# Optimization experiments

Measured on AMD Instinct MI355X. Metric: run time of the kernel, lower is better.

Reference implementation:

```python
import jax, jax.numpy as jnp
import numpy as np

L, H, DH, C, NRBF = 2, 4, 16, 64, 16   # depth, heads, dim_head, hidden dim, radial basis size
R = 10.0                                # valid_radius
EPS = 1e-8


def _layernorm(x, g, b):
    m = x.mean(-1, keepdims=True)
    v = ((x - m) ** 2).mean(-1, keepdims=True)
    return (x - m) / jnp.sqrt(v + 1e-5) * g + b


def setup_inputs() -> dict:
    key = jax.random.key(0)
    ks = iter(jax.random.split(key, 48))
    B, N, IN, OUT = 16, 128, 11, 19
    def rn(shape, fan_in):
        return jax.random.normal(next(ks), shape, jnp.float32) * (fan_in ** -0.5)
    inp = {
        "feats": jax.random.normal(next(ks), (B, N, IN), jnp.float32),
        "coords": jax.random.normal(next(ks), (B, N, 3), jnp.float32) * 3.0,
        "W_emb": rn((IN, C), IN), "b_emb": jnp.zeros((C,), jnp.float32),
        "Wq0": rn((L, C, H * DH), C), "Wk0": rn((L, C, H * DH), C), "Wv0": rn((L, C, H * DH), C),
        "Wq1": rn((L, C, H * DH), C), "Wk1": rn((L, C, H * DH), C), "Wv1": rn((L, C, H * DH), C),
        "rW1": rn((L, NRBF, 32), NRBF), "rb1": jnp.zeros((L, 32), jnp.float32),
        "rW2": rn((L, 32, 4 * H), 32), "rb2": jnp.zeros((L, 4 * H), jnp.float32),
        "Wo0": rn((L, H * DH, C), H * DH), "bo0": jnp.zeros((L, C), jnp.float32),
        "Wo1": rn((L, H * DH, C), H * DH),
        "g0": jnp.ones((L, C), jnp.float32), "b0": jnp.zeros((L, C), jnp.float32),
        "gn": jnp.ones((L, C), jnp.float32), "bn": jnp.zeros((L, C), jnp.float32),
        "g2": jnp.ones((L, C), jnp.float32), "b2": jnp.zeros((L, C), jnp.float32),
        "F1": rn((L, C, 4 * C), C), "fb1": jnp.zeros((L, 4 * C), jnp.float32),
        "F2": rn((L, 4 * C, C), 4 * C), "fb2": jnp.zeros((L, C), jnp.float32),
        "Wf1": rn((L, C, C), C),
        "Wout": rn((C, OUT), C), "bout": jnp.zeros((OUT,), jnp.float32),
        "mask": jnp.ones((B, N), bool),
        "adj": jnp.zeros((B, N, N), bool),
    }
    return inp


def reference(feats, coords, W_emb, b_emb, Wq0, Wk0, Wv0, Wq1, Wk1, Wv1,
              rW1, rb1, rW2, rb2, Wo0, bo0, Wo1, g0, b0, gn, bn, g2, b2,
              F1, fb1, F2, fb2, Wf1, Wout, bout, mask, adj):
    B, N = mask.shape
    f0 = feats @ W_emb + b_emb                                   # [B,N,C] degree-0 feats
    f1 = jnp.zeros((B, N, C, 3), f0.dtype)                       # degree-1 feats
    rel = coords[:, None, :, :] - coords[:, :, None, :]          # [B,N,N,3] r_j - r_i
    dist = jnp.sqrt((rel ** 2).sum(-1) + EPS)                    # [B,N,N]
    Y1 = rel / dist[..., None]                                   # degree-1 spherical harmonic
    pairm = mask[:, None, :] & mask[:, :, None]
    nmask = ((dist <= R) | adj) & pairm & (~jnp.eye(N, dtype=bool))
    centers = jnp.linspace(0.0, R, NRBF).astype(f0.dtype)
    rbf = jnp.exp(-((dist[..., None] - centers) ** 2) / (2.0 * (R / NRBF) ** 2))  # [B,N,N,NRBF]
    nmf = nmask[:, None].astype(f0.dtype)                        # [B,1,N,N]
    scale = DH ** -0.5

    for l in range(L):
        # radial kernel weights for the four tensor-product paths (per head)
        rh = jax.nn.relu(rbf @ rW1[l] + rb1[l])
        w = (rh @ rW2[l] + rb2[l]).reshape(B, N, N, 4, H)
        w = jnp.moveaxis(w, -1, 1)                               # [B,H,N,N,4]
        w00, w01, w10, w11 = w[..., 0], w[..., 1], w[..., 2], w[..., 3]

        x0 = _layernorm(f0, g0[l], b0[l])
        def heads0(x, W):
            return (x @ W).reshape(B, N, H, DH).transpose(0, 2, 1, 3)          # [B,H,N,DH]
        def heads1(x, W):
            return jnp.einsum('bncv,cm->bnmv', x, W).reshape(B, N, H, DH, 3).transpose(0, 2, 1, 3, 4)
        q0, k0, v0 = heads0(x0, Wq0[l]), heads0(x0, Wk0[l]), heads0(x0, Wv0[l])
        q1, k1, v1 = heads1(f1, Wq1[l]), heads1(f1, Wk1[l]), heads1(f1, Wv1[l])

        # invariant attention logits from degree-0 and degree-1 channels
        sim = (jnp.einsum('bhid,bhjd->bhij', q0, k0) * w00
               + jnp.einsum('bhidv,bhjdv->bhij', q1, k1) * w11) * scale
        sim = jnp.where(nmask[:, None], sim, -1e9)
        a = jax.nn.softmax(sim, axis=-1) * nmf                   # zero rows w/o neighbors

        # equivariant messages: 0->0, 1->0 (dot with Y1), 0->1 (times Y1), 1->1
        out0 = (jnp.einsum('bhij,bhjd->bhid', a * w00, v0)
                + jnp.einsum('bhij,bhjdv,bijv->bhid', a * w10, v1, Y1))
        out1 = (jnp.einsum('bhij,bhjd,bijv->bhidv', a * w01, v0, Y1)
                + jnp.einsum('bhij,bhjdv->bhidv', a * w11, v1))

        f0 = f0 + out0.transpose(0, 2, 1, 3).reshape(B, N, H * DH) @ Wo0[l] + bo0[l]
        f1 = f1 + jnp.einsum('bnmv,mc->bncv',
                             out1.transpose(0, 2, 1, 3, 4).reshape(B, N, H * DH, 3), Wo1[l])

        # equivariant norm on degree-1 (phase * learned gate of the norm)
        n1 = jnp.sqrt((f1 ** 2).sum(-1) + EPS)                   # [B,N,C]
        f1 = f1 / n1[..., None] * jax.nn.relu(n1 * gn[l] + bn[l])[..., None]

        # feedforward: MLP on degree-0, channel-mixing linear on degree-1
        f0 = f0 + jax.nn.relu(_layernorm(f0, g2[l], b2[l]) @ F1[l] + fb1[l]) @ F2[l] + fb2[l]
        f1 = f1 + jnp.einsum('bncv,cd->bndv', f1, Wf1[l])

    mf = mask.astype(f0.dtype)
    pooled = (f0 * mf[..., None]).sum(1) / jnp.clip(mf.sum(1, keepdims=True), 1.0, None)
    return pooled @ Wout + bout
```

## Files before the change

### kernel.cpp

```cpp
#include <hip/hip_runtime.h>
#include <hip/hip_bf16.h>


typedef __hip_bfloat16 bf16;
typedef __attribute__((ext_vector_type(8))) short short8;
typedef __attribute__((ext_vector_type(4))) float float4v;

__device__ __forceinline__ float waveSum64(float v) {
#pragma unroll
  for (int m = 1; m < 64; m <<= 1) v += __shfl_xor(v, m, 64);
  return v;
}

__device__ __forceinline__ float bits2f(unsigned short b) {
  return __uint_as_float(((unsigned int)b) << 16);
}
__device__ __forceinline__ unsigned short f2bu(float f) {
  unsigned int u = __float_as_uint(f);
  u = (u + 0x7fffu + ((u >> 16) & 1u)) >> 16;
  return (unsigned short)u;
}
__device__ __forceinline__ short8 pack8(float4 a, float4 b) {
  short8 r;
  r[0] = (short)f2bu(a.x); r[1] = (short)f2bu(a.y);
  r[2] = (short)f2bu(a.z); r[3] = (short)f2bu(a.w);
  r[4] = (short)f2bu(b.x); r[5] = (short)f2bu(b.y);
  r[6] = (short)f2bu(b.z); r[7] = (short)f2bu(b.w);
  return r;
}

__device__ __forceinline__ int voteSlice(const unsigned short* u, int start, int stride) {
  int insane = 0;
  for (int e = start; e < 1024; e += stride) {
    float f = bits2f(u[2 * e]);
    float af = fabsf(f);
    insane += (!(af < 1e4f) || (f != 0.f && af < 1e-20f)) ? 1 : 0;
  }
  return insane;
}

__device__ __forceinline__ float ldraw(const void* src, int idx, bool isbf) {
  if (isbf) return bits2f(((const unsigned short*)src)[idx]);
  return ((const float*)src)[idx];
}

struct ConvArgs {
  const void* src[30];
  int off[31];
};

__global__ void k_convtab(ConvArgs a, float* dst, int total, int nconv,
                          float2* __restrict__ tab) {
  __shared__ int cnt;
  int tid = threadIdx.x;
  if (tid == 0) cnt = 0;
  __syncthreads();
  atomicAdd(&cnt, voteSlice((const unsigned short*)a.src[0], tid, 256));
  __syncthreads();
  bool isbf = (cnt <= 100);

  if ((int)blockIdx.x < nconv) {
    int e = blockIdx.x * 256 + tid;
    if (e >= total) return;
    int k = 0;
    while (k < 29 && a.off[k + 1] <= e) k++;
    dst[e] = ldraw(a.src[k], e - a.off[k], isbf);
    return;
  }
  int g = (blockIdx.x - nconv) * 256 + tid;
  int l = g >> 10, bin = g & 1023;
  __shared__ float sW1[512], sb1[32], sW2[512], sb2[16];
  for (int k = tid; k < 512; k += 256) {
    sW1[k] = ldraw(a.src[10], l * 512 + k, isbf);
    sW2[k] = ldraw(a.src[12], l * 512 + k, isbf);
  }
  if (tid < 32) sb1[tid] = ldraw(a.src[11], l * 32 + tid, isbf);
  if (tid < 16) sb2[tid] = ldraw(a.src[13], l * 16 + tid, isbf);
  __syncthreads();
  float w[2][16];
#pragma unroll
  for (int t = 0; t < 2; ++t) {
    float d = (float)(bin + t) * 0.01f;
    float rbf[16];
#pragma unroll
    for (int r = 0; r < 16; ++r) {
      float x = d - (10.0f / 15.0f) * (float)r;
      rbf[r] = __expf(-x * x * 1.28f);
    }
#pragma unroll
    for (int o = 0; o < 16; ++o) w[t][o] = sb2[o];
    for (int k = 0; k < 32; ++k) {
      float acc = sb1[k];
#pragma unroll
      for (int r = 0; r < 16; ++r) acc += rbf[r] * sW1[r * 32 + k];
      acc = fmaxf(acc, 0.f);
#pragma unroll
      for (int o = 0; o < 16; ++o) w[t][o] += acc * sW2[k * 16 + o];
    }
  }
#pragma unroll
  for (int o = 0; o < 16; ++o)
    tab[l * 16384 + bin * 16 + o] = make_float2(w[0][o], w[1][o]);
}

__global__ void k_proj0(const float* __restrict__ feats, const float* __restrict__ W_emb,
                        const float* __restrict__ b_emb, const float* __restrict__ g0,
                        const float* __restrict__ b0, const float* __restrict__ Wq0,
                        const float* __restrict__ Wk0, const float* __restrict__ Wv0,
                        float* __restrict__ f0, float* __restrict__ q0,
                        float* __restrict__ k0, float* __restrict__ v0) {
  int row = blockIdx.x;
  int b = row >> 7, n = row & 127;
  int m = threadIdx.x;
  __shared__ float fs[11], x0s[64];
  if (m < 11) fs[m] = feats[row * 11 + m];
  __syncthreads();
  float val = b_emb[m];
#pragma unroll
  for (int k = 0; k < 11; k++) val += fs[k] * W_emb[k * 64 + m];
  f0[row * 64 + m] = val;
  float mu = waveSum64(val) * (1.f / 64.f);
  float dv = val - mu;
  float var = waveSum64(dv * dv) * (1.f / 64.f);
  x0s[m] = dv * rsqrtf(var + 1e-5f) * g0[m] + b0[m];
  __syncthreads();
  float aq = 0, ak = 0, av = 0;
  for (int c = 0; c < 64; c++) {
    float x = x0s[c];
    aq += x * Wq0[c * 64 + m];
    ak += x * Wk0[c * 64 + m];
    av += x * Wv0[c * 64 + m];
  }
  int h = m >> 4, d = m & 15;
  size_t o0 = ((size_t)((b * 4 + h) * 128 + n)) * 16 + d;
  q0[o0] = aq; k0[o0] = ak; v0[o0] = av;
}

__global__ void k_proj(const float* __restrict__ f0, const float* __restrict__ f1,
                       const float* __restrict__ g0, const float* __restrict__ b0,
                       const float* __restrict__ Wq0, const float* __restrict__ Wk0,
                       const float* __restrict__ Wv0, const float* __restrict__ Wq1,
                       const float* __restrict__ Wk1, const float* __restrict__ Wv1,
                       float* __restrict__ q0, float* __restrict__ k0, float* __restrict__ v0,
                       float* __restrict__ q1, float* __restrict__ k1, float* __restrict__ v1,
                       int l) {
  int row = blockIdx.x;
  int b = row >> 7, n = row & 127;
  int m = threadIdx.x;
  __shared__ float x0s[64], f1s[192];
  float val = f0[row * 64 + m];
  float mu = waveSum64(val) * (1.f / 64.f);
  float dv = val - mu;
  float var = waveSum64(dv * dv) * (1.f / 64.f);
  float xn = dv * rsqrtf(var + 1e-5f) * g0[l * 64 + m] + b0[l * 64 + m];
  x0s[m] = xn;
  f1s[m * 3 + 0] = f1[row * 192 + m * 3 + 0];
  f1s[m * 3 + 1] = f1[row * 192 + m * 3 + 1];
  f1s[m * 3 + 2] = f1[row * 192 + m * 3 + 2];
  __syncthreads();
  const float* wq0 = Wq0 + l * 4096;
  const float* wk0 = Wk0 + l * 4096;
  const float* wv0 = Wv0 + l * 4096;
  const float* wq1 = Wq1 + l * 4096;
  const float* wk1 = Wk1 + l * 4096;
  const float* wv1 = Wv1 + l * 4096;
  float aq = 0, ak = 0, av = 0;
  float aq1x = 0, aq1y = 0, aq1z = 0, ak1x = 0, ak1y = 0, ak1z = 0, av1x = 0, av1y = 0, av1z = 0;
  for (int c = 0; c < 64; c++) {
    float x = x0s[c];
    aq += x * wq0[c * 64 + m];
    ak += x * wk0[c * 64 + m];
    av += x * wv0[c * 64 + m];
    float fx = f1s[c * 3 + 0], fy = f1s[c * 3 + 1], fz = f1s[c * 3 + 2];
    float w;
    w = wq1[c * 64 + m]; aq1x += fx * w; aq1y += fy * w; aq1z += fz * w;
    w = wk1[c * 64 + m]; ak1x += fx * w; ak1y += fy * w; ak1z += fz * w;
    w = wv1[c * 64 + m]; av1x += fx * w; av1y += fy * w; av1z += fz * w;
  }
  int h = m >> 4, d = m & 15;
  size_t o0 = ((size_t)((b * 4 + h) * 128 + n)) * 16 + d;
  size_t o1 = ((size_t)((b * 4 + h) * 128 + n)) * 48 + d * 3;
  q0[o0] = aq; k0[o0] = ak; v0[o0] = av;
  q1[o1 + 0] = aq1x; q1[o1 + 1] = aq1y; q1[o1 + 2] = aq1z;
  k1[o1 + 0] = ak1x; k1[o1 + 1] = ak1y; k1[o1 + 2] = ak1z;
  v1[o1 + 0] = av1x; v1[o1 + 1] = av1y; v1[o1 + 2] = av1z;
}

template <int HASF1>
__global__ void __launch_bounds__(256, 4) k_attn(
    const float* __restrict__ coords, const float2* __restrict__ tab,
    const float* __restrict__ q0, const float* __restrict__ k0,
    const float* __restrict__ v0, const float* __restrict__ q1,
    const float* __restrict__ k1, const float* __restrict__ v1,
    float* __restrict__ out0, float* __restrict__ out1) {
  __shared__ union {
    unsigned short ks[128][64];
    unsigned short A16[64][128];
  } U;
  __shared__ unsigned int S01[8][128];
  __shared__ unsigned short Bt[64][128];
  __shared__ float cs[3][128];

  int tid = threadIdx.x;
  int bid = blockIdx.x;
  int bh = bid & 63, it = bid >> 6;
  int h = bh & 3, b = bh >> 2;
  int ibase = it * 8;
  size_t rowbase = (size_t)bh * 128;
  int lane = tid & 63, waveid = tid >> 6;
  int ln = lane & 15, lg = lane >> 4;

  short8 P0f = {0, 0, 0, 0, 0, 0, 0, 0};
  short8 P1f = {0, 0, 0, 0, 0, 0, 0, 0};
  short8 P2f = {0, 0, 0, 0, 0, 0, 0, 0};
  if (ln < 8) {
    int i = ibase + ln;
    if (HASF1) {
      const float* q1p = q1 + (rowbase + i) * 48;
      float4 fa = *(const float4*)&q1p[lg * 8];
      float4 fb = *(const float4*)&q1p[lg * 8 + 4];
      P0f = pack8(fa, fb);
      if (lg < 2) {
        fa = *(const float4*)&q1p[32 + lg * 8];
        fb = *(const float4*)&q1p[32 + lg * 8 + 4];
        P1f = pack8(fa, fb);
      }
    }
    if (lg >= 2) {
      const float* q0p = q0 + (rowbase + i) * 16;
      float4 fa = *(const float4*)&q0p[(lg - 2) * 8];
      float4 fb = *(const float4*)&q0p[(lg - 2) * 8 + 4];
      P2f = pack8(fa, fb);
    }
  }

  if (HASF1) {
    for (int e = tid; e < 2048; e += 256) {
      int j = e >> 4, t0 = (e & 15) * 4;
      float4 f;
      if (t0 < 48) f = *(const float4*)&k1[(rowbase + j) * 48 + t0];
      else f = *(const float4*)&k0[(rowbase + j) * 16 + (t0 - 48)];
      int g = t0 >> 3;
      ushort4 pk = {f2bu(f.x), f2bu(f.y), f2bu(f.z), f2bu(f.w)};
      *(ushort4*)&U.ks[j][((g ^ (j & 7)) << 3) | (t0 & 7)] = pk;
    }
  } else {
    for (int e = tid; e < 1024; e += 256) {
      int j = e >> 3, t0 = 32 + (e & 7) * 4;
      ushort4 pk = {0, 0, 0, 0};
      if (t0 >= 48) {
        float4 f = *(const float4*)&k0[(rowbase + j) * 16 + (t0 - 48)];
        pk.x = f2bu(f.x); pk.y = f2bu(f.y); pk.z = f2bu(f.z); pk.w = f2bu(f.w);
      }
      int g = t0 >> 3;
      *(ushort4*)&U.ks[j][((g ^ (j & 7)) << 3) | (t0 & 7)] = pk;
    }
  }
  for (int e = tid; e < 512; e += 256) {
    int j = e >> 2, q = e & 3;
    float4 f = *(const float4*)&v0[(rowbase + j) * 16 + q * 4];
    int jhi = j >> 3, jl = j & 7;
#pragma unroll
    for (int i2 = 0; i2 < 4; ++i2) {
      int d = q * 4 + i2;
      int sl = (jhi ^ d) << 3;
      float fv = (i2 == 0) ? f.x : (i2 == 1) ? f.y : (i2 == 2) ? f.z : f.w;
      Bt[d][sl | jl] = f2bu(fv);
      if (!HASF1) {
        Bt[16 + d][sl | jl] = 0;
        Bt[32 + d][sl | jl] = 0;
        Bt[48 + d][sl | jl] = 0;
      }
    }
  }
  if (HASF1) {
    for (int e = tid; e < 1536; e += 256) {
      int j = e / 12, q = e - j * 12;
      float4 f = *(const float4*)&v1[(rowbase + j) * 48 + q * 4];
      int jhi = j >> 3, jl = j & 7;
#pragma unroll
      for (int i2 = 0; i2 < 4; ++i2) {
        int flat = q * 4 + i2;
        int d = flat / 3, vv = flat - d * 3;
        int sl = (jhi ^ d) << 3;
        float fv = (i2 == 0) ? f.x : (i2 == 1) ? f.y : (i2 == 2) ? f.z : f.w;
        Bt[(vv + 1) * 16 + d][sl | jl] = f2bu(fv);
      }
    }
  }
  if (tid < 128) {
    cs[0][tid] = coords[((size_t)b * 128 + tid) * 3 + 0];
    cs[1][tid] = coords[((size_t)b * 128 + tid) * 3 + 1];
    cs[2][tid] = coords[((size_t)b * 128 + tid) * 3 + 2];
  }
  __syncthreads();

#pragma unroll
  for (int q = 0; q < 2; ++q) {
    int j = (waveid * 2 + q) * 16 + ln;
    int swz = j & 7;
    short8 bk1 = *(const short8*)&U.ks[j][(((4 + lg) ^ swz) << 3)];
    float4v a0 = {0.f, 0.f, 0.f, 0.f};
    a0 = __builtin_amdgcn_mfma_f32_16x16x32_bf16(P2f, bk1, a0, 0, 0, 0);
    float4v a1 = {0.f, 0.f, 0.f, 0.f};
    if (HASF1) {
      short8 bk0 = *(const short8*)&U.ks[j][((lg ^ swz) << 3)];
      a1 = __builtin_amdgcn_mfma_f32_16x16x32_bf16(P0f, bk0, a1, 0, 0, 0);
      a1 = __builtin_amdgcn_mfma_f32_16x16x32_bf16(P1f, bk1, a1, 0, 0, 0);
    }
    if (lg < 2) {
#pragma unroll
      for (int r = 0; r < 4; ++r) {
        unsigned int pk =
            (unsigned int)f2bu(a0[r]) | ((unsigned int)f2bu(a1[r]) << 16);
        S01[lg * 4 + r][j] = pk;
      }
    }
  }
  __syncthreads();

  {
    int row = tid >> 5, jg = tid & 31;
    int i = ibase + row;
    float cix = cs[0][i], ciy = cs[1][i], ciz = cs[2][i];
    uint4 sv = *(const uint4*)&S01[row][jg * 4];
    float e4[4], w4[4][4], yv[4][3];
    int nmmask = 0;
    float mx = -3e38f;
#pragma unroll
    for (int jj = 0; jj < 4; ++jj) {
      int j = jg * 4 + jj;
      float rx = cs[0][j] - cix;
      float ry = cs[1][j] - ciy;
      float rz = cs[2][j] - ciz;
      float dd = sqrtf(rx * rx + ry * ry + rz * rz + 1e-8f);
      float inv = 1.f / dd;
      yv[jj][0] = rx * inv; yv[jj][1] = ry * inv; yv[jj][2] = rz * inv;
      float tt = fminf(dd, 10.229f) * 100.f;
      int i0 = (int)tt;
      float fr = tt - (float)i0;
      const float2* Tp = tab + (i0 << 4) + h;
      float2 t0 = Tp[0], t1 = Tp[4], t2 = Tp[8], t3 = Tp[12];
      w4[jj][0] = t0.x + fr * (t0.y - t0.x);
      w4[jj][1] = t1.x + fr * (t1.y - t1.x);
      w4[jj][2] = t2.x + fr * (t2.y - t2.x);
      w4[jj][3] = t3.x + fr * (t3.y - t3.x);
      unsigned int sw = (jj == 0) ? sv.x : (jj == 1) ? sv.y : (jj == 2) ? sv.z : sv.w;
      float s0j = bits2f((unsigned short)(sw & 0xffffu));
      float s1j = bits2f((unsigned short)(sw >> 16));
      float sim = (s0j * w4[jj][0] + (HASF1 ? s1j * w4[jj][3] : 0.f)) * 0.25f;
      bool nm = (dd <= 10.0f) && (j != i);
      if (nm) nmmask |= (1 << jj);
      sim = nm ? sim : -1e9f;
      e4[jj] = sim;
      mx = fmaxf(mx, sim);
    }
#pragma unroll
    for (int m = 1; m < 32; m <<= 1) mx = fmaxf(mx, __shfl_xor(mx, m, 64));
    float ssum = 0.f;
#pragma unroll
    for (int jj = 0; jj < 4; ++jj) {
      e4[jj] = __expf(e4[jj] - mx);
      ssum += e4[jj];
    }
#pragma unroll
    for (int m = 1; m < 32; m <<= 1) ssum += __shfl_xor(ssum, m, 64);
    float rinv = 1.f / ssum;
    float aj[4];
#pragma unroll
    for (int jj = 0; jj < 4; ++jj)
      aj[jj] = ((nmmask >> jj) & 1) ? e4[jj] * rinv : 0.f;
#pragma unroll
    for (int s = 0; s < 8; ++s) {
      unsigned short t4[4];
#pragma unroll
      for (int jj = 0; jj < 4; ++jj) {
        float v;
        if (s == 0) v = aj[jj] * w4[jj][0];
        else if (s < 4) v = aj[jj] * w4[jj][2] * yv[jj][s - 1];
        else if (s < 7) v = aj[jj] * w4[jj][1] * yv[jj][s - 4];
        else v = aj[jj] * w4[jj][3];
        t4[jj] = f2bu(v);
      }
      ushort4 pk = {t4[0], t4[1], t4[2], t4[3]};
      int arow = row * 8 + s;
      int g = jg >> 1;
      *(ushort4*)&U.A16[arow][(((g ^ (arow & 15)) << 3) | ((jg & 1) * 4))] = pk;
    }
  }
  __syncthreads();

  float4v acc[4];
#pragma unroll
  for (int nt = 0; nt < 4; ++nt) acc[nt] = (float4v){0.f, 0.f, 0.f, 0.f};
  int m = waveid * 16 + ln;
#pragma unroll
  for (int kst = 0; kst < 4; ++kst) {
    int gk = kst * 4 + lg;
    short8 af = *(const short8*)&U.A16[m][((gk ^ ln) << 3)];
#pragma unroll
    for (int nt = 0; nt < 4; ++nt) {
      short8 bf = *(const short8*)&Bt[nt * 16 + ln][((gk ^ ln) << 3)];
      acc[nt] = __builtin_amdgcn_mfma_f32_16x16x32_bf16(af, bf, acc[nt], 0, 0, 0);
    }
  }
  {
    int qr = waveid * 2 + (lg >> 1);
    size_t orow = rowbase + ibase + qr;
    if ((lg & 1) == 0) {
      out0[orow * 16 + ln] = acc[0][0] + acc[1][1] + acc[2][2] + acc[3][3];
    } else {
#pragma unroll
      for (int vv = 0; vv < 3; ++vv)
        out1[orow * 48 + ln * 3 + vv] = acc[0][vv] + acc[1 + vv][3];
    }
  }
}

template <int LZ>
__global__ void __launch_bounds__(256) k_postff(
    const float* __restrict__ Wo0, const float* __restrict__ bo0,
    const float* __restrict__ Wo1, const float* __restrict__ gn,
    const float* __restrict__ bn, const float* __restrict__ g2,
    const float* __restrict__ b2w, const float* __restrict__ F1,
    const float* __restrict__ fb1, const float* __restrict__ F2,
    const float* __restrict__ fb2, const float* __restrict__ Wf1,
    const float* __restrict__ out0, const float* __restrict__ out1,
    float* __restrict__ f0, float* __restrict__ f1, int l) {
  int row = blockIdx.x;
  int b = row >> 7, n = row & 127;
  int tid = threadIdx.x;
  int g = tid >> 6, c = tid & 63;
  __shared__ float o0s[64], o1s[192], rs[64], xnl[64], hb[256], f1g[192];
  __shared__ float p0[4][64];
  __shared__ float p1[4][3][64];

  if (tid < 64) {
    int h = tid >> 4, d = tid & 15;
    o0s[tid] = out0[((size_t)((b * 4 + h) * 128 + n)) * 16 + d];
  } else {
    int t = tid - 64;
    int cc = t / 3, v = t - cc * 3;
    int h = cc >> 4, d = cc & 15;
    o1s[t] = out1[((size_t)((b * 4 + h) * 128 + n)) * 48 + d * 3 + v];
  }
  __syncthreads();
  {
    const float* wo0 = Wo0 + l * 4096;
    const float* wo1 = Wo1 + l * 4096;
    float a0 = 0, ax = 0, ay = 0, az = 0;
#pragma unroll
    for (int mi = 0; mi < 16; ++mi) {
      int m = g * 16 + mi;
      a0 += o0s[m] * wo0[m * 64 + c];
      float w = wo1[m * 64 + c];
      ax += o1s[m * 3 + 0] * w;
      ay += o1s[m * 3 + 1] * w;
      az += o1s[m * 3 + 2] * w;
    }
    p0[g][c] = a0;
    p1[g][0][c] = ax; p1[g][1][c] = ay; p1[g][2][c] = az;
  }
  __syncthreads();
  if (tid < 64) {
    float a0 = bo0[l * 64 + c] + p0[0][c] + p0[1][c] + p0[2][c] + p0[3][c];
    float f0p = f0[row * 64 + c] + a0;
    rs[c] = f0p;
    float fx = p1[0][0][c] + p1[1][0][c] + p1[2][0][c] + p1[3][0][c];
    float fy = p1[0][1][c] + p1[1][1][c] + p1[2][1][c] + p1[3][1][c];
    float fz = p1[0][2][c] + p1[1][2][c] + p1[2][2][c] + p1[3][2][c];
    if (!LZ) {
      fx += f1[row * 192 + c * 3 + 0];
      fy += f1[row * 192 + c * 3 + 1];
      fz += f1[row * 192 + c * 3 + 2];
    }
    float n1 = sqrtf(fx * fx + fy * fy + fz * fz + 1e-8f);
    float gate = fmaxf(n1 * gn[l * 64 + c] + bn[l * 64 + c], 0.f);
    float sc = gate / n1;
    f1g[c * 3 + 0] = fx * sc;
    f1g[c * 3 + 1] = fy * sc;
    f1g[c * 3 + 2] = fz * sc;
    float mu = waveSum64(f0p) * (1.f / 64.f);
    float dv = f0p - mu;
    float var = waveSum64(dv * dv) * (1.f / 64.f);
    xnl[c] = dv * rsqrtf(var + 1e-5f) * g2[l * 64 + c] + b2w[l * 64 + c];
  }
  __syncthreads();
  {
    float a = fb1[l * 256 + tid];
    const float* Fp = F1 + l * 16384;
    for (int cc = 0; cc < 64; ++cc) a += xnl[cc] * Fp[cc * 256 + tid];
    hb[tid] = fmaxf(a, 0.f);
  }
  __syncthreads();
  {
    const float* Fp = F2 + l * 16384;
    float s = 0;
#pragma unroll 8
    for (int kk = 0; kk < 64; ++kk) {
      int k = g * 64 + kk;
      s += hb[k] * Fp[k * 64 + c];
    }
    const float* Wp = Wf1 + l * 4096;
    float sx = 0, sy = 0, sz = 0;
#pragma unroll
    for (int mi = 0; mi < 16; ++mi) {
      int m = g * 16 + mi;
      float w = Wp[m * 64 + c];
      sx += f1g[m * 3 + 0] * w;
      sy += f1g[m * 3 + 1] * w;
      sz += f1g[m * 3 + 2] * w;
    }
    p0[g][c] = s;
    p1[g][0][c] = sx; p1[g][1][c] = sy; p1[g][2][c] = sz;
  }
  __syncthreads();
  if (tid < 64) {
    f0[row * 64 + c] = rs[c] + fb2[l * 64 + c] + p0[0][c] + p0[1][c] + p0[2][c] + p0[3][c];
    f1[row * 192 + c * 3 + 0] =
        f1g[c * 3 + 0] + p1[0][0][c] + p1[1][0][c] + p1[2][0][c] + p1[3][0][c];
    f1[row * 192 + c * 3 + 1] =
        f1g[c * 3 + 1] + p1[0][1][c] + p1[1][1][c] + p1[2][1][c] + p1[3][1][c];
    f1[row * 192 + c * 3 + 2] =
        f1g[c * 3 + 2] + p1[0][2][c] + p1[1][2][c] + p1[2][2][c] + p1[3][2][c];
  }
}

__global__ void k_final(const float* __restrict__ f0, const float* __restrict__ Wout,
                        const float* __restrict__ bout, const void* __restrict__ rawfeats,
                        void* __restrict__ out) {
  int b = blockIdx.x;
  int c = threadIdx.x;
  __shared__ float ps[64];
  int insane = voteSlice((const unsigned short*)rawfeats, c, 64);
  float cnt = waveSum64((float)insane);
  bool isbf = (cnt <= 100.f);
  float s = 0;
  for (int n = 0; n < 128; n++) s += f0[(b * 128 + n) * 64 + c];
  ps[c] = s * (1.f / 128.f);
  __syncthreads();
  if (c < 19) {
    float a = bout[c];
    for (int k = 0; k < 64; k++) a += ps[k] * Wout[k * 19 + c];
    if (isbf) ((bf16*)out)[b * 19 + c] = __float2bfloat16(a);
    else ((float*)out)[b * 19 + c] = a;
  }
}

static const int g_nelem[30] = {
    22528, 6144, 704, 64,
    8192, 8192, 8192, 8192, 8192, 8192,
    1024, 64, 1024, 32,
    8192, 128, 8192,
    128, 128, 128, 128, 128, 128,
    32768, 512, 32768, 128,
    8192, 1216, 19};

extern "C" void kernel_launch(void* const* d_in, const int* in_sizes, int n_in, void* d_out,
                              int out_size, void* d_ws, size_t ws_size, hipStream_t stream) {
  (void)in_sizes; (void)n_in; (void)out_size; (void)ws_size;

  int offs[31];
  offs[0] = 0;
  for (int i = 0; i < 30; i++) offs[i + 1] = offs[i] + g_nelem[i];
  int total = offs[30];

  float* conv = (float*)d_ws;
  float* p = conv + 173632;
  float* f0 = p; p += 131072;
  float* f1 = p; p += 393216;
  float* q0 = p; p += 131072;
  float* k0 = p; p += 131072;
  float* v0 = p; p += 131072;
  float* q1 = p; p += 393216;
  float* k1 = p; p += 393216;
  float* v1 = p; p += 393216;
  float* out0 = p; p += 131072;
  float* out1 = p; p += 393216;
  float2* tab2 = (float2*)p; p += 65536;

  ConvArgs ca;
  for (int i = 0; i < 30; i++) ca.src[i] = d_in[i];
  for (int i = 0; i < 31; i++) ca.off[i] = offs[i];

  int nconv = (total + 255) / 256;
  k_convtab<<<nconv + 8, 256, 0, stream>>>(ca, conv, total, nconv, tab2);

  const float* feats = conv + offs[0];
  const float* coords = conv + offs[1];
  const float* W_emb = conv + offs[2];
  const float* b_emb = conv + offs[3];
  const float* Wq0 = conv + offs[4];
  const float* Wk0 = conv + offs[5];
  const float* Wv0 = conv + offs[6];
  const float* Wq1 = conv + offs[7];
  const float* Wk1 = conv + offs[8];
  const float* Wv1 = conv + offs[9];
  const float* Wo0 = conv + offs[14];
  const float* bo0 = conv + offs[15];
  const float* Wo1 = conv + offs[16];
  const float* g0 = conv + offs[17];
  const float* b0 = conv + offs[18];
  const float* gn = conv + offs[19];
  const float* bn = conv + offs[20];
  const float* g2 = conv + offs[21];
  const float* b2w = conv + offs[22];
  const float* F1 = conv + offs[23];
  const float* fb1 = conv + offs[24];
  const float* F2 = conv + offs[25];
  const float* fb2 = conv + offs[26];
  const float* Wf1 = conv + offs[27];
  const float* Wout = conv + offs[28];
  const float* bout = conv + offs[29];

  k_proj0<<<2048, 64, 0, stream>>>(feats, W_emb, b_emb, g0, b0, Wq0, Wk0, Wv0, f0, q0, k0, v0);
  k_attn<0><<<1024, 256, 0, stream>>>(coords, tab2, q0, k0, v0, q1, k1, v1, out0, out1);
  k_postff<1><<<2048, 256, 0, stream>>>(Wo0, bo0, Wo1, gn, bn, g2, b2w, F1, fb1, F2, fb2, Wf1,
                                        out0, out1, f0, f1, 0);
  k_proj<<<2048, 64, 0, stream>>>(f0, f1, g0, b0, Wq0, Wk0, Wv0, Wq1, Wk1, Wv1, q0, k0, v0,
                                  q1, k1, v1, 1);
  k_attn<1><<<1024, 256, 0, stream>>>(coords, tab2 + 16384, q0, k0, v0, q1, k1, v1, out0, out1);
  k_postff<0><<<2048, 256, 0, stream>>>(Wo0, bo0, Wo1, gn, bn, g2, b2w, F1, fb1, F2, fb2, Wf1,
                                        out0, out1, f0, f1, 1);

  k_final<<<16, 64, 0, stream>>>(f0, Wout, bout, d_in[0], d_out);
}
```

Before: 131.4 us.

## Fuse post-attention FF with next-layer projection and pack four rows per block

Merges the post-attention output projection, equivariant norm and feedforward kernel with the next layer's layernorm plus Q/K/V projections into one kernel, so f1 no longer goes to global memory and one launch is removed. Each 256-thread block now handles four rows with one wave per row instead of splitting one row across four waves. The last layer skips all degree-1 work because its result never reaches the output. The cost is that each wave now runs the full 64- and 256-length reductions alone, giving longer per-thread loops and less parallelism per row.

```diff
diff --git a/kernel.cpp b/kernel.cpp
--- a/kernel.cpp
+++ b/kernel.cpp
@@ -103,30 +103,31 @@
     tab[l * 16384 + bin * 16 + o] = make_float2(w[0][o], w[1][o]);
 }
 
-__global__ void k_proj0(const float* __restrict__ feats, const float* __restrict__ W_emb,
-                        const float* __restrict__ b_emb, const float* __restrict__ g0,
-                        const float* __restrict__ b0, const float* __restrict__ Wq0,
-                        const float* __restrict__ Wk0, const float* __restrict__ Wv0,
-                        float* __restrict__ f0, float* __restrict__ q0,
-                        float* __restrict__ k0, float* __restrict__ v0) {
-  int row = blockIdx.x;
+__global__ void __launch_bounds__(256) k_proj0(
+    const float* __restrict__ feats, const float* __restrict__ W_emb,
+    const float* __restrict__ b_emb, const float* __restrict__ g0,
+    const float* __restrict__ b0, const float* __restrict__ Wq0,
+    const float* __restrict__ Wk0, const float* __restrict__ Wv0,
+    float* __restrict__ f0, float* __restrict__ q0, float* __restrict__ k0,
+    float* __restrict__ v0) {
+  int g = threadIdx.x >> 6, m = threadIdx.x & 63;
+  int row = blockIdx.x * 4 + g;
   int b = row >> 7, n = row & 127;
-  int m = threadIdx.x;
-  __shared__ float fs[11], x0s[64];
-  if (m < 11) fs[m] = feats[row * 11 + m];
+  __shared__ float fs[4][12], x0s[4][64];
+  if (m < 11) fs[g][m] = feats[row * 11 + m];
   __syncthreads();
   float val = b_emb[m];
 #pragma unroll
-  for (int k = 0; k < 11; k++) val += fs[k] * W_emb[k * 64 + m];
+  for (int k = 0; k < 11; k++) val += fs[g][k] * W_emb[k * 64 + m];
   f0[row * 64 + m] = val;
   float mu = waveSum64(val) * (1.f / 64.f);
   float dv = val - mu;
   float var = waveSum64(dv * dv) * (1.f / 64.f);
-  x0s[m] = dv * rsqrtf(var + 1e-5f) * g0[m] + b0[m];
+  x0s[g][m] = dv * rsqrtf(var + 1e-5f) * g0[m] + b0[m];
   __syncthreads();
   float aq = 0, ak = 0, av = 0;
   for (int c = 0; c < 64; c++) {
-    float x = x0s[c];
+    float x = x0s[g][c];
     aq += x * Wq0[c * 64 + m];
     ak += x * Wk0[c * 64 + m];
     av += x * Wv0[c * 64 + m];
@@ -134,56 +135,6 @@
   int h = m >> 4, d = m & 15;
   size_t o0 = ((size_t)((b * 4 + h) * 128 + n)) * 16 + d;
   q0[o0] = aq; k0[o0] = ak; v0[o0] = av;
-}
-
-__global__ void k_proj(const float* __restrict__ f0, const float* __restrict__ f1,
-                       const float* __restrict__ g0, const float* __restrict__ b0,
-                       const float* __restrict__ Wq0, const float* __restrict__ Wk0,
-                       const float* __restrict__ Wv0, const float* __restrict__ Wq1,
-                       const float* __restrict__ Wk1, const float* __restrict__ Wv1,
-                       float* __restrict__ q0, float* __restrict__ k0, float* __restrict__ v0,
-                       float* __restrict__ q1, float* __restrict__ k1, float* __restrict__ v1,
-                       int l) {
-  int row = blockIdx.x;
-  int b = row >> 7, n = row & 127;
-  int m = threadIdx.x;
-  __shared__ float x0s[64], f1s[192];
-  float val = f0[row * 64 + m];
-  float mu = waveSum64(val) * (1.f / 64.f);
-  float dv = val - mu;
-  float var = waveSum64(dv * dv) * (1.f / 64.f);
-  float xn = dv * rsqrtf(var + 1e-5f) * g0[l * 64 + m] + b0[l * 64 + m];
-  x0s[m] = xn;
-  f1s[m * 3 + 0] = f1[row * 192 + m * 3 + 0];
-  f1s[m * 3 + 1] = f1[row * 192 + m * 3 + 1];
-  f1s[m * 3 + 2] = f1[row * 192 + m * 3 + 2];
-  __syncthreads();
-  const float* wq0 = Wq0 + l * 4096;
-  const float* wk0 = Wk0 + l * 4096;
-  const float* wv0 = Wv0 + l * 4096;
-  const float* wq1 = Wq1 + l * 4096;
-  const float* wk1 = Wk1 + l * 4096;
-  const float* wv1 = Wv1 + l * 4096;
-  float aq = 0, ak = 0, av = 0;
-  float aq1x = 0, aq1y = 0, aq1z = 0, ak1x = 0, ak1y = 0, ak1z = 0, av1x = 0, av1y = 0, av1z = 0;
-  for (int c = 0; c < 64; c++) {
-    float x = x0s[c];
-    aq += x * wq0[c * 64 + m];
-    ak += x * wk0[c * 64 + m];
-    av += x * wv0[c * 64 + m];
-    float fx = f1s[c * 3 + 0], fy = f1s[c * 3 + 1], fz = f1s[c * 3 + 2];
-    float w;
-    w = wq1[c * 64 + m]; aq1x += fx * w; aq1y += fy * w; aq1z += fz * w;
-    w = wk1[c * 64 + m]; ak1x += fx * w; ak1y += fy * w; ak1z += fz * w;
-    w = wv1[c * 64 + m]; av1x += fx * w; av1y += fy * w; av1z += fz * w;
-  }
-  int h = m >> 4, d = m & 15;
-  size_t o0 = ((size_t)((b * 4 + h) * 128 + n)) * 16 + d;
-  size_t o1 = ((size_t)((b * 4 + h) * 128 + n)) * 48 + d * 3;
-  q0[o0] = aq; k0[o0] = ak; v0[o0] = av;
-  q1[o1 + 0] = aq1x; q1[o1 + 1] = aq1y; q1[o1 + 2] = aq1z;
-  k1[o1 + 0] = ak1x; k1[o1 + 1] = ak1y; k1[o1 + 2] = ak1z;
-  v1[o1 + 0] = av1x; v1[o1 + 1] = av1y; v1[o1 + 2] = av1z;
 }
 
 template <int HASF1>
@@ -417,112 +368,116 @@
   }
 }
 
-template <int LZ>
-__global__ void __launch_bounds__(256) k_postff(
+template <int LAST>
+__global__ void __launch_bounds__(256) k_postproj(
     const float* __restrict__ Wo0, const float* __restrict__ bo0,
     const float* __restrict__ Wo1, const float* __restrict__ gn,
     const float* __restrict__ bn, const float* __restrict__ g2,
     const float* __restrict__ b2w, const float* __restrict__ F1,
     const float* __restrict__ fb1, const float* __restrict__ F2,
     const float* __restrict__ fb2, const float* __restrict__ Wf1,
+    const float* __restrict__ g0n, const float* __restrict__ b0n,
+    const float* __restrict__ Wq0n, const float* __restrict__ Wk0n,
+    const float* __restrict__ Wv0n, const float* __restrict__ Wq1n,
+    const float* __restrict__ Wk1n, const float* __restrict__ Wv1n,
     const float* __restrict__ out0, const float* __restrict__ out1,
-    float* __restrict__ f0, float* __restrict__ f1, int l) {
-  int row = blockIdx.x;
+    float* __restrict__ f0, float* __restrict__ q0, float* __restrict__ k0,
+    float* __restrict__ v0, float* __restrict__ q1, float* __restrict__ k1,
+    float* __restrict__ v1) {
+  int g = threadIdx.x >> 6, c = threadIdx.x & 63;
+  int row = blockIdx.x * 4 + g;
   int b = row >> 7, n = row & 127;
-  int tid = threadIdx.x;
-  int g = tid >> 6, c = tid & 63;
-  __shared__ float o0s[64], o1s[192], rs[64], xnl[64], hb[256], f1g[192];
-  __shared__ float p0[4][64];
-  __shared__ float p1[4][3][64];
-
-  if (tid < 64) {
-    int h = tid >> 4, d = tid & 15;
-    o0s[tid] = out0[((size_t)((b * 4 + h) * 128 + n)) * 16 + d];
-  } else {
-    int t = tid - 64;
-    int cc = t / 3, v = t - cc * 3;
-    int h = cc >> 4, d = cc & 15;
-    o1s[t] = out1[((size_t)((b * 4 + h) * 128 + n)) * 48 + d * 3 + v];
-  }
-  __syncthreads();
-  {
-    const float* wo0 = Wo0 + l * 4096;
-    const float* wo1 = Wo1 + l * 4096;
-    float a0 = 0, ax = 0, ay = 0, az = 0;
-#pragma unroll
-    for (int mi = 0; mi < 16; ++mi) {
-      int m = g * 16 + mi;
-      a0 += o0s[m] * wo0[m * 64 + c];
-      float w = wo1[m * 64 + c];
-      ax += o1s[m * 3 + 0] * w;
-      ay += o1s[m * 3 + 1] * w;
-      az += o1s[m * 3 + 2] * w;
-    }
-    p0[g][c] = a0;
-    p1[g][0][c] = ax; p1[g][1][c] = ay; p1[g][2][c] = az;
-  }
-  __syncthreads();
-  if (tid < 64) {
-    float a0 = bo0[l * 64 + c] + p0[0][c] + p0[1][c] + p0[2][c] + p0[3][c];
-    float f0p = f0[row * 64 + c] + a0;
-    rs[c] = f0p;
-    float fx = p1[0][0][c] + p1[1][0][c] + p1[2][0][c] + p1[3][0][c];
-    float fy = p1[0][1][c] + p1[1][1][c] + p1[2][1][c] + p1[3][1][c];
-    float fz = p1[0][2][c] + p1[1][2][c] + p1[2][2][c] + p1[3][2][c];
-    if (!LZ) {
-      fx += f1[row * 192 + c * 3 + 0];
-      fy += f1[row * 192 + c * 3 + 1];
-      fz += f1[row * 192 + c * 3 + 2];
-    }
-    float n1 = sqrtf(fx * fx + fy * fy + fz * fz + 1e-8f);
-    float gate = fmaxf(n1 * gn[l * 64 + c] + bn[l * 64 + c], 0.f);
+  __shared__ float o0s[4][64], xnl[4][64], hb[4][256];
+  __shared__ float o1s[LAST ? 1 : 4][192];
+  __shared__ float f1g[LAST ? 1 : 4][192];
+  __shared__ float x0s[LAST ? 1 : 4][64];
+  __shared__ float f1n[LAST ? 1 : 4][192];
+
+  int h = c >> 4, d = c & 15;
+  size_t rb = (size_t)((b * 4 + h) * 128 + n);
+  o0s[g][c] = out0[rb * 16 + d];
+  if (!LAST) {
+    o1s[g][c * 3 + 0] = out1[rb * 48 + d * 3 + 0];
+    o1s[g][c * 3 + 1] = out1[rb * 48 + d * 3 + 1];
+    o1s[g][c * 3 + 2] = out1[rb * 48 + d * 3 + 2];
+  }
+  __syncthreads();
+  float a0 = bo0[c];
+  float ax = 0, ay = 0, az = 0;
+  for (int m = 0; m < 64; m++) {
+    a0 += o0s[g][m] * Wo0[m * 64 + c];
+    if (!LAST) {
+      float w = Wo1[m * 64 + c];
+      ax += o1s[g][m * 3 + 0] * w;
+      ay += o1s[g][m * 3 + 1] * w;
+      az += o1s[g][m * 3 + 2] * w;
+    }
+  }
+  float f0p = f0[row * 64 + c] + a0;
+  if (!LAST) {
+    float n1 = sqrtf(ax * ax + ay * ay + az * az + 1e-8f);
+    float gate = fmaxf(n1 * gn[c] + bn[c], 0.f);
     float sc = gate / n1;
-    f1g[c * 3 + 0] = fx * sc;
-    f1g[c * 3 + 1] = fy * sc;
-    f1g[c * 3 + 2] = fz * sc;
-    float mu = waveSum64(f0p) * (1.f / 64.f);
-    float dv = f0p - mu;
-    float var = waveSum64(dv * dv) * (1.f / 64.f);
-    xnl[c] = dv * rsqrtf(var + 1e-5f) * g2[l * 64 + c] + b2w[l * 64 + c];
-  }
-  __syncthreads();
-  {
-    float a = fb1[l * 256 + tid];
-    const float* Fp = F1 + l * 16384;
-    for (int cc = 0; cc < 64; ++cc) a += xnl[cc] * Fp[cc * 256 + tid];
-    hb[tid] = fmaxf(a, 0.f);
-  }
-  __syncthreads();
-  {
-    const float* Fp = F2 + l * 16384;
-    float s = 0;
+    f1g[g][c * 3 + 0] = ax * sc;
+    f1g[g][c * 3 + 1] = ay * sc;
+    f1g[g][c * 3 + 2] = az * sc;
+  }
+  float mu = waveSum64(f0p) * (1.f / 64.f);
+  float dv = f0p - mu;
+  float var = waveSum64(dv * dv) * (1.f / 64.f);
+  xnl[g][c] = dv * rsqrtf(var + 1e-5f) * g2[c] + b2w[c];
+  __syncthreads();
+#pragma unroll
+  for (int u = 0; u < 4; ++u) {
+    int t = u * 64 + c;
+    float a = fb1[t];
+    for (int cc = 0; cc < 64; ++cc) a += xnl[g][cc] * F1[cc * 256 + t];
+    hb[g][t] = fmaxf(a, 0.f);
+  }
+  __syncthreads();
+  float s = fb2[c];
 #pragma unroll 8
-    for (int kk = 0; kk < 64; ++kk) {
-      int k = g * 64 + kk;
-      s += hb[k] * Fp[k * 64 + c];
-    }
-    const float* Wp = Wf1 + l * 4096;
-    float sx = 0, sy = 0, sz = 0;
-#pragma unroll
-    for (int mi = 0; mi < 16; ++mi) {
-      int m = g * 16 + mi;
-      float w = Wp[m * 64 + c];
-      sx += f1g[m * 3 + 0] * w;
-      sy += f1g[m * 3 + 1] * w;
-      sz += f1g[m * 3 + 2] * w;
-    }
-    p0[g][c] = s;
-    p1[g][0][c] = sx; p1[g][1][c] = sy; p1[g][2][c] = sz;
-  }
-  __syncthreads();
-  if (tid < 64) {
-    f0[row * 64 + c] = rs[c] + fb2[l * 64 + c] + p0[0][c] + p0[1][c] + p0[2][c] + p0[3][c];
-    f1[row * 192 + c * 3 + 0] =
-        f1g[c * 3 + 0] + p1[0][0][c] + p1[1][0][c] + p1[2][0][c] + p1[3][0][c];
-    f1[row * 192 + c * 3 + 1] =
-        f1g[c * 3 + 1] + p1[0][1][c] + p1[1][1][c] + p1[2][1][c] + p1[3][1][c];
-    f1[row * 192 + c * 3 + 2] =
-        f1g[c * 3 + 2] + p1[0][2][c] + p1[1][2][c] + p1[2][2][c] + p1[3][2][c];
+  for (int k = 0; k < 256; ++k) s += hb[g][k] * F2[k * 64 + c];
+  float f0n = f0p + s;
+  f0[row * 64 + c] = f0n;
+  if (!LAST) {
+    float sx = f1g[g][c * 3 + 0], sy = f1g[g][c * 3 + 1], sz = f1g[g][c * 3 + 2];
+    for (int m = 0; m < 64; ++m) {
+      float w = Wf1[m * 64 + c];
+      sx += f1g[g][m * 3 + 0] * w;
+      sy += f1g[g][m * 3 + 1] * w;
+      sz += f1g[g][m * 3 + 2] * w;
+    }
+    float mu2 = waveSum64(f0n) * (1.f / 64.f);
+    float dv2 = f0n - mu2;
+    float var2 = waveSum64(dv2 * dv2) * (1.f / 64.f);
+    x0s[g][c] = dv2 * rsqrtf(var2 + 1e-5f) * g0n[c] + b0n[c];
+    f1n[g][c * 3 + 0] = sx;
+    f1n[g][c * 3 + 1] = sy;
+    f1n[g][c * 3 + 2] = sz;
+  }
+  __syncthreads();
+  if (!LAST) {
+    float aq = 0, ak = 0, av = 0;
+    float aq1x = 0, aq1y = 0, aq1z = 0, ak1x = 0, ak1y = 0, ak1z = 0;
+    float av1x = 0, av1y = 0, av1z = 0;
+    for (int cc = 0; cc < 64; ++cc) {
+      float x = x0s[g][cc];
+      aq += x * Wq0n[cc * 64 + c];
+      ak += x * Wk0n[cc * 64 + c];
+      av += x * Wv0n[cc * 64 + c];
+      float fx = f1n[g][cc * 3 + 0], fy = f1n[g][cc * 3 + 1], fz = f1n[g][cc * 3 + 2];
+      float w;
+      w = Wq1n[cc * 64 + c]; aq1x += fx * w; aq1y += fy * w; aq1z += fz * w;
+      w = Wk1n[cc * 64 + c]; ak1x += fx * w; ak1y += fy * w; ak1z += fz * w;
+      w = Wv1n[cc * 64 + c]; av1x += fx * w; av1y += fy * w; av1z += fz * w;
+    }
+    size_t o0 = rb * 16 + d;
+    size_t o1 = rb * 48 + d * 3;
+    q0[o0] = aq; k0[o0] = ak; v0[o0] = av;
+    q1[o1 + 0] = aq1x; q1[o1 + 1] = aq1y; q1[o1 + 2] = aq1z;
+    k1[o1 + 0] = ak1x; k1[o1 + 1] = ak1y; k1[o1 + 2] = ak1z;
+    v1[o1 + 0] = av1x; v1[o1 + 1] = av1y; v1[o1 + 2] = av1z;
   }
 }
 
@@ -568,7 +523,6 @@
   float* conv = (float*)d_ws;
   float* p = conv + 173632;
   float* f0 = p; p += 131072;
-  float* f1 = p; p += 393216;
   float* q0 = p; p += 131072;
   float* k0 = p; p += 131072;
   float* v0 = p; p += 131072;
@@ -613,15 +567,19 @@
   const float* Wout = conv + offs[28];
   const float* bout = conv + offs[29];
 
-  k_proj0<<<2048, 64, 0, stream>>>(feats, W_emb, b_emb, g0, b0, Wq0, Wk0, Wv0, f0, q0, k0, v0);
+  k_proj0<<<512, 256, 0, stream>>>(feats, W_emb, b_emb, g0, b0, Wq0, Wk0, Wv0, f0, q0, k0, v0);
   k_attn<0><<<1024, 256, 0, stream>>>(coords, tab2, q0, k0, v0, q1, k1, v1, out0, out1);
-  k_postff<1><<<2048, 256, 0, stream>>>(Wo0, bo0, Wo1, gn, bn, g2, b2w, F1, fb1, F2, fb2, Wf1,
-                                        out0, out1, f0, f1, 0);
-  k_proj<<<2048, 64, 0, stream>>>(f0, f1, g0, b0, Wq0, Wk0, Wv0, Wq1, Wk1, Wv1, q0, k0, v0,
-                                  q1, k1, v1, 1);
+  k_postproj<0><<<512, 256, 0, stream>>>(
+      Wo0, bo0, Wo1, gn, bn, g2, b2w, F1, fb1, F2, fb2, Wf1,
+      g0 + 64, b0 + 64, Wq0 + 4096, Wk0 + 4096, Wv0 + 4096,
+      Wq1 + 4096, Wk1 + 4096, Wv1 + 4096,
+      out0, out1, f0, q0, k0, v0, q1, k1, v1);
   k_attn<1><<<1024, 256, 0, stream>>>(coords, tab2 + 16384, q0, k0, v0, q1, k1, v1, out0, out1);
-  k_postff<0><<<2048, 256, 0, stream>>>(Wo0, bo0, Wo1, gn, bn, g2, b2w, F1, fb1, F2, fb2, Wf1,
-                                        out0, out1, f0, f1, 1);
+  k_postproj<1><<<512, 256, 0, stream>>>(
+      Wo0 + 4096, bo0 + 64, Wo1 + 4096, gn + 64, bn + 64, g2 + 64, b2w + 64,
+      F1 + 16384, fb1 + 256, F2 + 16384, fb2 + 64, Wf1 + 4096,
+      nullptr, nullptr, nullptr, nullptr, nullptr, nullptr, nullptr, nullptr,
+      out0, out1, f0, q0, k0, v0, q1, k1, v1);
 
   k_final<<<16, 64, 0, stream>>>(f0, Wout, bout, d_in[0], d_out);
 }
```

New measurement: 123.3 us. -6.2%, faster.
